# Optimization experiments

Hardware: AMD Instinct MI355X
Metric: run time of the kernel (lower is better)

## Reference

```python
import jax, jax.numpy as jnp
import numpy as np

N_PAIR = 45  # n_agents=10 -> 10*9/2
TINY_THR = np.sqrt(np.finfo(np.float32).tiny).astype(np.float32) * N_PAIR


def setup_inputs() -> dict:
    key = jax.random.key(0)
    ks = jax.random.split(key, 8)
    bs, T, din, H = 4096, 64, 512, 64
    s = lambda fan: 1.0 / np.sqrt(fan)
    return {
        "main": jax.random.normal(ks[0], (1, bs, T, din), jnp.float32),
        "hidden_states": jnp.zeros((1, bs, 1, H), jnp.float32),
        "epsilons": jax.random.uniform(ks[1], (bs, 1), jnp.float32),
        "W_fc1": jax.random.normal(ks[2], (H, din), jnp.float32) * s(din),
        "b_fc1": jnp.zeros((H,), jnp.float32),
        "W_ih": jax.random.normal(ks[3], (3 * H, H), jnp.float32) * s(H),
        "W_hh": jax.random.normal(ks[4], (3 * H, H), jnp.float32) * s(H),
        "b_ih": jnp.zeros((3 * H,), jnp.float32),
        "b_hh": jnp.zeros((3 * H,), jnp.float32),
        "W_out": jax.random.normal(ks[5], (N_PAIR, H), jnp.float32) * s(H),
        "b_out": jnp.zeros((N_PAIR,), jnp.float32),
    }


def reference(main, hidden_states, epsilons, W_fc1, b_fc1, W_ih, W_hh, b_ih, b_hh, W_out, b_out):
    x = main[0]                       # [bs, T, din]
    h0 = hidden_states[0, :, 0, :]    # [bs, H]
    H = h0.shape[-1]

    # Encoder: fc1 + relu (time-independent, fully batched)
    enc = jax.nn.relu(jnp.einsum('bti,oi->bto', x, W_fc1) + b_fc1)  # [bs,T,H]
    # Precompute input-side GRU gates for all timesteps
    gi = jnp.einsum('bth,gh->btg', enc, W_ih) + b_ih                # [bs,T,3H]
    gi_t = jnp.transpose(gi, (1, 0, 2))                             # [T,bs,3H]

    def step(h, g_in):
        gh = h @ W_hh.T + b_hh
        i_r, i_z, i_n = jnp.split(g_in, 3, axis=-1)
        h_r, h_z, h_n = jnp.split(gh, 3, axis=-1)
        r = jax.nn.sigmoid(i_r + h_r)
        z = jax.nn.sigmoid(i_z + h_z)
        n = jnp.tanh(i_n + r * h_n)
        h_new = (1.0 - z) * n + z * h
        return h_new, h_new

    _, hs = jax.lax.scan(step, h0, gi_t)          # hs: [T,bs,H]
    hs = jnp.transpose(hs, (1, 0, 2))             # [bs,T,H]

    # Output head + custom exp-normalize with zero-sum guard
    logits = jnp.einsum('bth,oh->bto', hs, W_out) + b_out  # [bs,T,N_PAIR]
    p = jnp.exp(logits)
    p_sum = jnp.sum(p, axis=-1, keepdims=True)
    p_sum = jnp.where(p_sum <= TINY_THR, 1.0, p_sum)
    p = p / p_sum

    # Epsilon-greedy mixing (softmax exploration, not test_mode)
    eps = epsilons[:, None, :]                    # [bs,1,1]
    p = eps / N_PAIR + p * (1.0 - eps)

    x_out = p[None]                               # [1,bs,T,N_PAIR]
    h_out = hs[None]                              # [1,bs,T,H]
    return (x_out, h_out)
```

## Files before the change

### kernel.cpp

```cpp
#include <hip/hip_runtime.h>

typedef __attribute__((ext_vector_type(4))) float  f32x4;
typedef __attribute__((ext_vector_type(4))) __bf16 bf16x4;
typedef __attribute__((ext_vector_type(8))) __bf16 bf16x8;

#define MFMA16 __builtin_amdgcn_mfma_f32_16x16x32_bf16
#define TINY_THR 4.8789098e-18f
#define XOUT_N ((size_t)4096 * 64 * 45)

__device__ __forceinline__ void bar_lds() {
  asm volatile("s_waitcnt lgkmcnt(0)\n\ts_barrier" ::: "memory");
}
__device__ __forceinline__ void split_bf16(float v, __bf16& h, __bf16& l) {
  h = (__bf16)v; l = (__bf16)(v - (float)h);
}
__device__ __forceinline__ void gll16(const void* g, void* l) {
  __builtin_amdgcn_global_load_lds(
      (const __attribute__((address_space(1))) void*)g,
      (__attribute__((address_space(3))) void*)l, 16, 0, 0);
}

__device__ __forceinline__ int pk_off(int row, int col) {
  const int kk = col >> 5, rem = col & 31;
  const int half = rem >> 4, qq = (rem >> 2) & 3, j = rem & 3;
  return row * 128 + ((((kk << 2) | qq) ^ (row & 7)) << 4) + half * 8 + j * 2;
}
__device__ __forceinline__ bf16x8 frag_pk(const char* base, int row, int kk, int qq) {
  return *(const bf16x8*)(base + row * 128 + ((((kk << 2) | qq) ^ (row & 7)) << 4));
}

__global__ void k_prepW(const float* __restrict__ Wfc, __bf16* __restrict__ Wpk) {
  const int idx = blockIdx.x * 256 + threadIdx.x;
  const float v = Wfc[idx];
  __bf16 h, l; split_bf16(v, h, l);
  const int row = idx >> 9, k = idx & 511;
  const int c = k >> 6, kl = k & 63;
  const int kk = kl >> 5, rem = kl & 31;
  const int half = rem >> 4, q = (rem >> 2) & 3, j = rem & 3;
  const int blk = ((kk << 2) | q) ^ (row & 7);
  const int pos = c * 8192 + row * 64 + blk * 8 + half * 4 + j;
  Wpk[pos] = h;
  Wpk[pos + 4096] = l;
}

__global__ __launch_bounds__(256, 2) void k_encgemm(
    const float* __restrict__ x, const __bf16* __restrict__ Wpk,
    const float* __restrict__ bfc, __bf16* __restrict__ pairs) {
  __shared__ __attribute__((aligned(16))) char sm[65536];
  const int tid  = threadIdx.x;
  const int lane = tid & 63;
  const int wv   = tid >> 6;
  const int fr   = lane & 15;
  const int q    = lane >> 4;
  const int b    = blockIdx.x;

  auto stage = [&](int c, int buf) {
    char* xbase = sm + buf * 16384;
    char* wbase = sm + 32768 + buf * 16384;
    #pragma unroll
    for (int i = 0; i < 4; ++i) {
      const int B   = wv * 256 + i * 64 + lane;
      const int row = B >> 4, blk = B & 15;
      const int bp  = blk ^ (row & 15);
      const int colb = ((bp >> 3) << 5) | ((bp & 1) << 4) | (((bp >> 1) & 3) << 2);
      const float* src = x + ((size_t)b * 64 + row) * 512 + c * 64 + colb;
      gll16(src, xbase + wv * 4096 + i * 1024);
    }
    #pragma unroll
    for (int i = 0; i < 4; ++i) {
      const __bf16* srcw = Wpk + c * 8192 + wv * 2048 + i * 512 + lane * 8;
      gll16(srcw, wbase + wv * 4096 + i * 1024);
    }
  };

  f32x4 acc[4];
  #pragma unroll
  for (int nt = 0; nt < 4; ++nt) acc[nt] = (f32x4){0.f, 0.f, 0.f, 0.f};

  stage(0, 0);
  int buf = 0;
  for (int c = 0; c < 8; ++c) {
    if (c < 7) {
      stage(c + 1, buf ^ 1);
      asm volatile("s_waitcnt vmcnt(8)\n\ts_barrier" ::: "memory");
    } else {
      asm volatile("s_waitcnt vmcnt(0)\n\ts_barrier" ::: "memory");
    }
    const char* xbase = sm + buf * 16384;
    const char* wbase = sm + 32768 + buf * 16384;
    const int arow = wv * 16 + fr;
    bf16x8 Ah[2], Al[2];
    #pragma unroll
    for (int kk = 0; kk < 2; ++kk) {
      f32x4 u0 = *(const f32x4*)(xbase + arow * 256 + (((kk * 8 + q * 2 + 0) ^ (arow & 15)) << 4));
      f32x4 u1 = *(const f32x4*)(xbase + arow * 256 + (((kk * 8 + q * 2 + 1) ^ (arow & 15)) << 4));
      #pragma unroll
      for (int j = 0; j < 4; ++j) {
        __bf16 h, l;
        split_bf16(u0[j], h, l); Ah[kk][j] = h;     Al[kk][j] = l;
        split_bf16(u1[j], h, l); Ah[kk][4 + j] = h; Al[kk][4 + j] = l;
      }
    }
    #pragma unroll
    for (int nt = 0; nt < 4; ++nt) {
      const int brow = nt * 16 + fr;
      #pragma unroll
      for (int kk = 0; kk < 2; ++kk) {
        bf16x8 Bh = frag_pk(wbase, brow, kk, q);
        bf16x8 Bl = frag_pk(wbase + 8192, brow, kk, q);
        acc[nt] = MFMA16(Ah[kk], Bh, acc[nt], 0, 0, 0);
        acc[nt] = MFMA16(Ah[kk], Bl, acc[nt], 0, 0, 0);
        acc[nt] = MFMA16(Al[kk], Bh, acc[nt], 0, 0, 0);
      }
    }
    bar_lds();
    buf ^= 1;
  }
  float* ep = (float*)(sm + wv * 4352);
  #pragma unroll
  for (int nt = 0; nt < 4; ++nt) {
    const int o = nt * 16 + fr;
    const float bb = bfc[o];
    #pragma unroll
    for (int e = 0; e < 4; ++e)
      ep[(q * 4 + e) * 68 + o] = fmaxf(acc[nt][e] + bb, 0.f);
  }
  asm volatile("s_waitcnt lgkmcnt(0)" ::: "memory");
  const int r = b & 15;
  const size_t bgbase = (size_t)(b >> 4) * 64 * 4096;
  #pragma unroll
  for (int r2 = 0; r2 < 4; ++r2) {
    const int row = (lane >> 4) + 4 * r2;
    const int cg  = lane & 15;
    f32x4 v = *(const f32x4*)(ep + row * 68 + cg * 4);
    bf16x4 hi4, lo4;
    #pragma unroll
    for (int j = 0; j < 4; ++j) {
      __bf16 h, l; split_bf16(v[j], h, l); hi4[j] = h; lo4[j] = l;
    }
    const int blk  = ((((cg >> 3) << 2) | (cg & 3)) ^ (r & 7));
    const int boff = r * 128 + (blk << 4) + ((cg >> 2) & 1) * 8;
    char* dst = (char*)pairs + bgbase + (size_t)(wv * 16 + row) * 4096 + boff;
    *(bf16x4*)dst = hi4;
    *(bf16x4*)(dst + 2048) = lo4;
  }
}

__global__ __launch_bounds__(512, 1) void k_scan(
    const __bf16* __restrict__ pairs, const float* __restrict__ h0g,
    const float* __restrict__ eps, const float* __restrict__ Wih,
    const float* __restrict__ Whh, const float* __restrict__ bih,
    const float* __restrict__ bhh, const float* __restrict__ Wout,
    const float* __restrict__ bout, float* __restrict__ xout,
    float* __restrict__ hout) {
  __shared__ __attribute__((aligned(16))) char sm[55808];
  char* const wst0 = sm;
  char* const wst1 = sm + 24576;

  const int tid  = threadIdx.x;
  const int lane = tid & 63;
  const int wv   = tid >> 6;
  const int fr   = lane & 15;
  const int q    = lane >> 4;
  const int bbase = blockIdx.x * 16;
  const bool isB = (wv < 4);
  const int aw  = wv - 4;
  const int at  = tid & 255;
  const int sb  = at >> 4;
  const int sub = at & 15;

  float biasNh = 0.f;
  int hcol = 0;
  float boutv = 0.f, epsv = 0.f;
  if (isB) {
    hcol = wv * 16 + fr;
    biasNh = bhh[128 + hcol];
  } else {
    const int gc = aw * 16 + fr;
    if (aw < 3) boutv = (gc < 45) ? bout[gc] : -1e30f;
    epsv = eps[bbase + sb];
  }
  float bR_ = 0.f, bZ_ = 0.f, bN_ = 0.f;
  if (!isB) {
    const int gc = aw * 16 + fr;
    bR_ = bih[gc] + bhh[gc];
    bZ_ = bih[64 + gc] + bhh[64 + gc];
    bN_ = bih[128 + gc];
  }

  bf16x8 Fh[3][2], Fl[3][2];
  bf16x8 Fout[2][2];

  for (int idx = tid; idx < 192 * 64; idx += 512) {
    __bf16 h, l; split_bf16(Wih[idx], h, l);
    const int off = pk_off(idx >> 6, idx & 63);
    *(__bf16*)(wst0 + off) = h;
    *(__bf16*)(wst1 + off) = l;
  }
  bar_lds();
  if (!isB) {
    #pragma unroll
    for (int t3 = 0; t3 < 3; ++t3)
      #pragma unroll
      for (int kk = 0; kk < 2; ++kk) {
        const int row = (aw + 4 * t3) * 16 + fr;
        Fh[t3][kk] = frag_pk(wst0, row, kk, q);
        Fl[t3][kk] = frag_pk(wst1, row, kk, q);
      }
  }
  bar_lds();
  for (int idx = tid; idx < 192 * 64; idx += 512) {
    __bf16 h, l; split_bf16(Whh[idx], h, l);
    const int off = pk_off(idx >> 6, idx & 63);
    *(__bf16*)(wst0 + off) = h;
    *(__bf16*)(wst1 + off) = l;
  }
  bar_lds();
  if (isB) {
    #pragma unroll
    for (int t3 = 0; t3 < 3; ++t3)
      #pragma unroll
      for (int kk = 0; kk < 2; ++kk) {
        const int row = (wv + 4 * t3) * 16 + fr;
        Fh[t3][kk] = frag_pk(wst0, row, kk, q);
        Fl[t3][kk] = frag_pk(wst1, row, kk, q);
      }
  }
  bar_lds();
  for (int idx = tid; idx < 48 * 64; idx += 512) {
    float v = (idx < 45 * 64) ? Wout[idx] : 0.f;
    __bf16 h, l; split_bf16(v, h, l);
    const int off = pk_off(idx >> 6, idx & 63);
    *(__bf16*)(wst0 + off) = h;
    *(__bf16*)(wst1 + off) = l;
  }
  bar_lds();
  if (!isB && aw < 3) {
    #pragma unroll
    for (int kk = 0; kk < 2; ++kk) {
      const int row = aw * 16 + fr;
      Fout[kk][0] = frag_pk(wst0, row, kk, q);
      Fout[kk][1] = frag_pk(wst1, row, kk, q);
    }
  }
  bar_lds();

  auto gate_mfma = [&](const char* s0, f32x4& a0, f32x4& a1, f32x4& a2) {
    const char* s1 = s0 + 2048;
    bf16x8 Sh[2], Sl[2];
    #pragma unroll
    for (int kk = 0; kk < 2; ++kk) {
      Sh[kk] = frag_pk(s0, fr, kk, q);
      Sl[kk] = frag_pk(s1, fr, kk, q);
    }
    __builtin_amdgcn_s_setprio(1);
    #pragma unroll
    for (int kk = 0; kk < 2; ++kk) {
      a0 = MFMA16(Sh[kk], Fh[0][kk], a0, 0, 0, 0);
      a0 = MFMA16(Sh[kk], Fl[0][kk], a0, 0, 0, 0);
      a0 = MFMA16(Sl[kk], Fh[0][kk], a0, 0, 0, 0);
      a1 = MFMA16(Sh[kk], Fh[1][kk], a1, 0, 0, 0);
      a1 = MFMA16(Sh[kk], Fl[1][kk], a1, 0, 0, 0);
      a1 = MFMA16(Sl[kk], Fh[1][kk], a1, 0, 0, 0);
      a2 = MFMA16(Sh[kk], Fh[2][kk], a2, 0, 0, 0);
      a2 = MFMA16(Sh[kk], Fl[2][kk], a2, 0, 0, 0);
      a2 = MFMA16(Sl[kk], Fh[2][kk], a2, 0, 0, 0);
    }
    __builtin_amdgcn_s_setprio(0);
  };
  auto stage_epd = [&](int dst, int tt) {
    const char* src = (const char*)pairs +
        ((size_t)blockIdx.x * 64 + tt) * 4096 + (at >> 7) * 2048 + (at & 127) * 16;
    char* dl = sm + 8192 + dst * 4096 + (at >> 7) * 2048 + (at & 127) * 16;
    gll16(src, dl);
  };
  auto put_gi = [&](int dst, const f32x4& a0, const f32x4& a1, const f32x4& a2) {
    float* gw = (float*)(sm + 16384 + dst * 16640);
    const int gc = aw * 16 + fr;
    #pragma unroll
    for (int e = 0; e < 4; ++e) {
      f32x4 o = (f32x4){a0[e] + bR_, a1[e] + bZ_, a2[e] + bN_, 0.f};
      *(f32x4*)(gw + (q * 4 + e) * 260 + gc * 4) = o;
    }
  };

  float hreg[4] = {0.f, 0.f, 0.f, 0.f};
  if (isB) {
    #pragma unroll
    for (int e = 0; e < 4; ++e)
      hreg[e] = h0g[(size_t)(bbase + q * 4 + e) * 64 + hcol];
    char* h0b = sm;
    char* h1b = sm + 2048;
    #pragma unroll
    for (int e = 0; e < 4; ++e) {
      __bf16 h, l; split_bf16(hreg[e], h, l);
      const int off = pk_off(q * 4 + e, hcol);
      *(__bf16*)(h0b + off) = h;
      *(__bf16*)(h1b + off) = l;
    }
  } else {
    stage_epd(1, 0);
    stage_epd(0, 1);
    asm volatile("s_waitcnt vmcnt(0)" ::: "memory");
  }
  bar_lds();
  if (!isB) {
    f32x4 a0 = (f32x4){0.f,0.f,0.f,0.f}, a1 = a0, a2 = a0;
    gate_mfma(sm + 8192 + 1 * 4096, a0, a1, a2);
    put_gi(0, a0, a1, a2);
  }
  bar_lds();

  auto body = [&](int t, int cur) {
    f32x4 a0 = (f32x4){0.f,0.f,0.f,0.f}, a1 = a0, a2 = a0;
    float giN[4];
    if (isB) {
      if (t <= 63) {
        const float* gr = (const float*)(sm + 16384 + cur * 16640);
        #pragma unroll
        for (int e = 0; e < 4; ++e) {
          f32x4 gv = *(const f32x4*)(gr + (q * 4 + e) * 260 + hcol * 4);
          a0[e] = gv[0]; a1[e] = gv[1]; giN[e] = gv[2];
        }
        gate_mfma(sm + cur * 4096, a0, a1, a2);
        char* n0 = sm + (cur ^ 1) * 4096;
        char* n1 = n0 + 2048;
        #pragma unroll
        for (int e = 0; e < 4; ++e) {
          const float rr = 1.f / (1.f + __expf(-a0[e]));
          const float zz = 1.f / (1.f + __expf(-a1[e]));
          const float npre = giN[e] + rr * (a2[e] + biasNh);
          const float nn = 2.f / (1.f + __expf(-2.f * npre)) - 1.f;
          const float hv = (1.f - zz) * nn + zz * hreg[e];
          hreg[e] = hv;
          hout[((size_t)(bbase + q * 4 + e) * 64 + t) * 64 + hcol] = hv;
          __bf16 h, l; split_bf16(hv, h, l);
          const int off = pk_off(q * 4 + e, hcol);
          *(__bf16*)(n0 + off) = h;
          *(__bf16*)(n1 + off) = l;
        }
      }
    } else {
      if (t <= 61) stage_epd(cur ^ 1, t + 2);
      if (t <= 62) {
        gate_mfma(sm + 8192 + cur * 4096, a0, a1, a2);
        put_gi(cur ^ 1, a0, a1, a2);
      }
      if (t >= 1 && t <= 64 && aw < 3) {
        const char* hp0c = sm + cur * 4096;
        const char* hp1c = hp0c + 2048;
        bf16x8 Hh[2], Hl[2];
        #pragma unroll
        for (int kk = 0; kk < 2; ++kk) {
          Hh[kk] = frag_pk(hp0c, fr, kk, q);
          Hl[kk] = frag_pk(hp1c, fr, kk, q);
        }
        f32x4 lacc = (f32x4){0.f, 0.f, 0.f, 0.f};
        #pragma unroll
        for (int kk = 0; kk < 2; ++kk) {
          lacc = MFMA16(Hh[kk], Fout[kk][0], lacc, 0, 0, 0);
          lacc = MFMA16(Hh[kk], Fout[kk][1], lacc, 0, 0, 0);
          lacc = MFMA16(Hl[kk], Fout[kk][0], lacc, 0, 0, 0);
        }
        float* lg = (float*)(sm + 49664 + (cur ^ 1) * 3072);
        #pragma unroll
        for (int e = 0; e < 4; ++e)
          lg[(q * 4 + e) * 48 + aw * 16 + fr] = lacc[e] + boutv;
      }
      if (t >= 2) {
        const float* lg = (const float*)(sm + 49664 + cur * 3072);
        const float e0 = __expf(lg[sb * 48 + sub]);
        const float e1 = __expf(lg[sb * 48 + sub + 16]);
        const float e2 = __expf(lg[sb * 48 + sub + 32]);
        float s = e0 + e1 + e2;
        s += __shfl_xor(s, 1, 16);
        s += __shfl_xor(s, 2, 16);
        s += __shfl_xor(s, 4, 16);
        s += __shfl_xor(s, 8, 16);
        if (s <= TINY_THR) s = 1.f;
        const float sc  = (1.f - epsv) / s;
        const float bse = epsv * (1.f / 45.f);
        float* orow = xout + ((size_t)(bbase + sb) * 64 + (t - 2)) * 45;
        orow[sub] = bse + e0 * sc;
        orow[sub + 16] = bse + e1 * sc;
        if (sub < 13) orow[sub + 32] = bse + e2 * sc;
      }
      if (t <= 61) {
        if (t >= 2) asm volatile("s_waitcnt vmcnt(3)" ::: "memory");
        else        asm volatile("s_waitcnt vmcnt(0)" ::: "memory");
      }
    }
    bar_lds();
  };

  for (int t2 = 0; t2 < 66; t2 += 2) {
    body(t2, 0);
    body(t2 + 1, 1);
  }
}

extern "C" void kernel_launch(void* const* d_in, const int* in_sizes, int n_in,
                              void* d_out, int out_size, void* d_ws, size_t ws_size,
                              hipStream_t stream) {
  (void)in_sizes; (void)n_in; (void)out_size; (void)ws_size;
  const float* x    = (const float*)d_in[0];
  const float* h0   = (const float*)d_in[1];
  const float* eps  = (const float*)d_in[2];
  const float* Wfc  = (const float*)d_in[3];
  const float* bfc  = (const float*)d_in[4];
  const float* Wih  = (const float*)d_in[5];
  const float* Whh  = (const float*)d_in[6];
  const float* bih  = (const float*)d_in[7];
  const float* bhh  = (const float*)d_in[8];
  const float* Wout = (const float*)d_in[9];
  const float* bout = (const float*)d_in[10];

  float* xout = (float*)d_out;
  float* hout = xout + XOUT_N;
  __bf16* pairs = (__bf16*)d_ws;
  __bf16* Wpk = (__bf16*)d_out;

  k_prepW<<<128, 256, 0, stream>>>(Wfc, Wpk);
  k_encgemm<<<4096, 256, 0, stream>>>(x, Wpk, bfc, pairs);
  k_scan<<<256, 512, 0, stream>>>(pairs, h0, eps, Wih, Whh, bih, bhh, Wout,
                                  bout, xout, hout);
}
```

Measured before the change: 237.2 us.

## Store encoder pairs batch-major and prefetch through registers instead of LDS DMA

The encoder kernel now writes each batch row's hi/lo bf16 split as one contiguous 16-byte packed vector per row, in a batch-major layout, instead of two swizzled 8-byte stores in a time-major layout. The scan kernel replaces its global-to-LDS DMA staging and explicit vmcnt waits with register prefetches issued two steps ahead. Each prefetch is unpacked into the swizzled LDS layout with ordinary ds writes. This is meant to give the encoder wider, more coalesced stores and to take global-load waits off the scan's critical path. The cost is extra VGPRs, extra LDS write instructions, and strided global reads in the scan (16 KB stride per batch row).

```diff
diff --git a/kernel.cpp b/kernel.cpp
--- a/kernel.cpp
+++ b/kernel.cpp
@@ -126,23 +126,18 @@
       ep[(q * 4 + e) * 68 + o] = fmaxf(acc[nt][e] + bb, 0.f);
   }
   asm volatile("s_waitcnt lgkmcnt(0)" ::: "memory");
-  const int r = b & 15;
-  const size_t bgbase = (size_t)(b >> 4) * 64 * 4096;
+  char* const pb = (char*)pairs + (size_t)b * 16384;
   #pragma unroll
   for (int r2 = 0; r2 < 4; ++r2) {
     const int row = (lane >> 4) + 4 * r2;
     const int cg  = lane & 15;
     f32x4 v = *(const f32x4*)(ep + row * 68 + cg * 4);
-    bf16x4 hi4, lo4;
+    bf16x8 pk;
     #pragma unroll
     for (int j = 0; j < 4; ++j) {
-      __bf16 h, l; split_bf16(v[j], h, l); hi4[j] = h; lo4[j] = l;
-    }
-    const int blk  = ((((cg >> 3) << 2) | (cg & 3)) ^ (r & 7));
-    const int boff = r * 128 + (blk << 4) + ((cg >> 2) & 1) * 8;
-    char* dst = (char*)pairs + bgbase + (size_t)(wv * 16 + row) * 4096 + boff;
-    *(bf16x4*)dst = hi4;
-    *(bf16x4*)(dst + 2048) = lo4;
+      __bf16 h, l; split_bf16(v[j], h, l); pk[j] = h; pk[4 + j] = l;
+    }
+    *(bf16x8*)(pb + (size_t)(wv * 16 + row) * 256 + cg * 16) = pk;
   }
 }
 
@@ -268,11 +263,22 @@
     }
     __builtin_amdgcn_s_setprio(0);
   };
-  auto stage_epd = [&](int dst, int tt) {
-    const char* src = (const char*)pairs +
-        ((size_t)blockIdx.x * 64 + tt) * 4096 + (at >> 7) * 2048 + (at & 127) * 16;
-    char* dl = sm + 8192 + dst * 4096 + (at >> 7) * 2048 + (at & 127) * 16;
-    gll16(src, dl);
+
+  const int r_  = at >> 4;
+  const int cg_ = at & 15;
+  const int blk_ = ((((cg_ >> 3) << 2) | (cg_ & 3)) ^ (r_ & 7));
+  const int epoff = r_ * 128 + (blk_ << 4) + ((cg_ >> 2) & 1) * 8;
+  const char* tile0 = (const char*)pairs +
+      (size_t)(bbase + r_) * 16384 + cg_ * 16;
+  auto load_pair = [&](int tt, bf16x8& v) {
+    v = *(const bf16x8*)(tile0 + tt * 256);
+  };
+  auto put_epd = [&](int dst, const bf16x8& v) {
+    char* dl = sm + 8192 + dst * 4096 + epoff;
+    bf16x4 hi = {v[0], v[1], v[2], v[3]};
+    bf16x4 lo = {v[4], v[5], v[6], v[7]};
+    *(bf16x4*)dl = hi;
+    *(bf16x4*)(dl + 2048) = lo;
   };
   auto put_gi = [&](int dst, const f32x4& a0, const f32x4& a1, const f32x4& a2) {
     float* gw = (float*)(sm + 16384 + dst * 16640);
@@ -285,6 +291,7 @@
   };
 
   float hreg[4] = {0.f, 0.f, 0.f, 0.f};
+  bf16x8 pvA, pvB;
   if (isB) {
     #pragma unroll
     for (int e = 0; e < 4; ++e)
@@ -299,9 +306,13 @@
       *(__bf16*)(h1b + off) = l;
     }
   } else {
-    stage_epd(1, 0);
-    stage_epd(0, 1);
-    asm volatile("s_waitcnt vmcnt(0)" ::: "memory");
+    bf16x8 v0_, v1_;
+    load_pair(0, v0_);
+    load_pair(1, v1_);
+    put_epd(1, v0_);
+    put_epd(0, v1_);
+    load_pair(2, pvA);
+    load_pair(3, pvB);
   }
   bar_lds();
   if (!isB) {
@@ -311,7 +322,7 @@
   }
   bar_lds();
 
-  auto body = [&](int t, int cur) {
+  auto body = [&](int t, int cur, bf16x8& pvC) {
     f32x4 a0 = (f32x4){0.f,0.f,0.f,0.f}, a1 = a0, a2 = a0;
     float giN[4];
     if (isB) {
@@ -341,7 +352,7 @@
         }
       }
     } else {
-      if (t <= 61) stage_epd(cur ^ 1, t + 2);
+      if (t <= 61) put_epd(cur ^ 1, pvC);
       if (t <= 62) {
         gate_mfma(sm + 8192 + cur * 4096, a0, a1, a2);
         put_gi(cur ^ 1, a0, a1, a2);
@@ -367,6 +378,7 @@
         for (int e = 0; e < 4; ++e)
           lg[(q * 4 + e) * 48 + aw * 16 + fr] = lacc[e] + boutv;
       }
+      if (t <= 59) load_pair(t + 4, pvC);
       if (t >= 2) {
         const float* lg = (const float*)(sm + 49664 + cur * 3072);
         const float e0 = __expf(lg[sb * 48 + sub]);
@@ -385,17 +397,13 @@
         orow[sub + 16] = bse + e1 * sc;
         if (sub < 13) orow[sub + 32] = bse + e2 * sc;
       }
-      if (t <= 61) {
-        if (t >= 2) asm volatile("s_waitcnt vmcnt(3)" ::: "memory");
-        else        asm volatile("s_waitcnt vmcnt(0)" ::: "memory");
-      }
     }
     bar_lds();
   };
 
   for (int t2 = 0; t2 < 66; t2 += 2) {
-    body(t2, 0);
-    body(t2 + 1, 1);
+    body(t2, 0, pvA);
+    body(t2 + 1, 1, pvB);
   }
 }
 
```

Result: no change. 238.8 us (+0.6%).
